# Performance work log

Hardware: AMD Instinct MI355X
Metric: run time of the kernel (lower is better)

Reference implementation:

```python
import jax, jax.numpy as jnp
from jax import lax
import numpy as np

K = 10            # size_feat
N_MU = 10         # number of mean-PSF components
NCH = K * K + N_MU  # 110 depthwise channels
KLEN = 65         # precomputed kernel length


def setup_inputs() -> dict:
    key = jax.random.key(0)
    ks = jax.random.split(key, 12)
    B, C, H, W = 1, 3, 256, 256
    img = jax.random.uniform(ks[0], (B, C, H, W), jnp.float32)
    zernike = jax.random.normal(ks[1], (B, H, W, 35), jnp.float32)
    # pos displacements (first 2 channels) scaled to a few pixels
    zernike = zernike.at[..., :2].multiply(2.0)
    fc1_w = jax.random.normal(ks[2], (200, 33), jnp.float32) / np.float32(np.sqrt(33))
    fc1_b = jax.random.normal(ks[3], (200,), jnp.float32) * 0.01
    fc2_w = jax.random.normal(ks[4], (200, 200), jnp.float32) / np.float32(np.sqrt(200))
    fc2_b = jax.random.normal(ks[5], (200,), jnp.float32) * 0.01
    fc3_w = jax.random.normal(ks[6], (100, 200), jnp.float32) * 0.01
    fc3_b = jnp.zeros((100,), jnp.float32)
    basis_left = jax.random.normal(ks[7], (KLEN, K), jnp.float32) * 0.05
    basis_right = jax.random.normal(ks[8], (KLEN, K), jnp.float32) * 0.05
    mu = jax.random.uniform(ks[9], (KLEN, N_MU), jnp.float32) / np.float32(KLEN)
    return dict(img=img, zernike=zernike, fc1_w=fc1_w, fc1_b=fc1_b,
                fc2_w=fc2_w, fc2_b=fc2_b, fc3_w=fc3_w, fc3_b=fc3_b,
                basis_left=basis_left, basis_right=basis_right, mu=mu, ksize=65)


def _grid_sample_border(img, pos):
    """Bilinear grid_sample, padding_mode='border', align_corners=False.
    img: (B,C,H,W), pos: (B,H,W,2) pixel displacements (x,y)."""
    B, C, H, W = img.shape
    yy, xx = jnp.meshgrid(jnp.arange(H, dtype=jnp.float32),
                          jnp.arange(W, dtype=jnp.float32), indexing='ij')
    grid = jnp.stack((xx, yy), -1)                       # (H,W,2)
    wh = jnp.array([W - 1, H - 1], jnp.float32)
    flow = 2.0 * (grid[None] + pos) / wh - 1.0           # (B,H,W,2) in [-1,1]
    ix = ((flow[..., 0] + 1.0) * W - 1.0) * 0.5
    iy = ((flow[..., 1] + 1.0) * H - 1.0) * 0.5
    ix = jnp.clip(ix, 0.0, W - 1)
    iy = jnp.clip(iy, 0.0, H - 1)
    x0 = jnp.floor(ix); y0 = jnp.floor(iy)
    wx = ix - x0;       wy = iy - y0
    x0i = jnp.clip(x0.astype(jnp.int32), 0, W - 1)
    y0i = jnp.clip(y0.astype(jnp.int32), 0, H - 1)
    x1i = jnp.clip(x0i + 1, 0, W - 1)
    y1i = jnp.clip(y0i + 1, 0, H - 1)

    def bilerp(im, x0i, x1i, y0i, y1i, wx, wy):
        g = lambda yi, xi: im[:, yi, xi]                 # (C,H,W)
        top = g(y0i, x0i) * (1 - wx) + g(y0i, x1i) * wx
        bot = g(y1i, x0i) * (1 - wx) + g(y1i, x1i) * wx
        return top * (1 - wy) + bot * wy

    return jax.vmap(bilerp)(img, x0i, x1i, y0i, y1i, wx, wy)


def _depthwise(x, w, pad_axis, pad):
    # x: (N, NCH, H, W); w: (NCH,1,kh,kw). Reflect 'same' padding on pad_axis.
    cfg = [(0, 0)] * 4
    cfg[pad_axis] = (pad, pad)
    xp = jnp.pad(x, cfg, mode='reflect')
    return lax.conv_general_dilated(
        xp, w, (1, 1), 'VALID',
        dimension_numbers=('NCHW', 'OIHW', 'NCHW'),
        feature_group_count=x.shape[1])


def _forward(img, zernike, fc1_w, fc1_b, fc2_w, fc2_b, fc3_w, fc3_b,
             basis_left, basis_right, mu, ksize):
    B, C, H, W = img.shape
    pad = ksize // 2
    # --- grid-sample warp ---
    tilt = _grid_sample_border(img, zernike[..., :2])    # (B,C,H,W)
    # --- per-pixel MLP -> PSF coefficients ---
    f = zernike[..., 2:]                                  # (B,H,W,33)
    h = jax.nn.leaky_relu(f @ fc1_w.T + fc1_b)
    h = jax.nn.leaky_relu(h @ fc2_w.T + fc2_b)
    coef = h @ fc3_w.T + fc3_b                            # (B,H,W,100)
    weight = jnp.concatenate(
        [coef, jnp.ones((B, H, W, N_MU), coef.dtype)], -1)  # (B,H,W,110)
    # --- elementwise weight multiply ---
    big = jnp.concatenate([tilt, jnp.ones_like(tilt)], 1)  # (B,2C,H,W)
    big = big[..., None] * weight[:, None]                 # (B,2C,H,W,110)
    x = big.reshape(B * 2 * C, H, W, NCH).transpose(0, 3, 1, 2)  # (B*2C,110,H,W)
    # --- separable depthwise blur kernels (outer products Z_i x X_j + mu) ---
    wl = jnp.concatenate([jnp.repeat(basis_left.T, K, axis=0), mu.T], 0)  # (110,klen)
    wr = jnp.concatenate([jnp.tile(basis_right.T, (K, 1)), mu.T], 0)      # (110,klen)
    wl = wl[:, None, :, None]                              # (110,1,klen,1)
    wr = wr[:, None, None, :]                              # (110,1,1,klen)
    y = _depthwise(x, wl, 2, pad)
    y = _depthwise(y, wr, 3, pad)
    d = y.reshape(B, 2 * C, NCH, H, W)
    out = jnp.sum(d[:, :3], axis=2) / jnp.sum(d[:, 3:], axis=2)  # (B,3,H,W)
    return out


def reference(img, zernike, fc1_w, fc1_b, fc2_w, fc2_b, fc3_w, fc3_b,
              basis_left, basis_right, mu, ksize):
    return _forward(img, zernike, fc1_w, fc1_b, fc2_w, fc2_b, fc3_w, fc3_b,
                    basis_left, basis_right, mu, ksize)
```

## Files before the change

### kernel.cpp

```cpp
#include <hip/hip_runtime.h>

#define HW 65536

typedef __attribute__((ext_vector_type(8))) short short8;
typedef __attribute__((ext_vector_type(4))) float float4v;

__device__ __forceinline__ int refl(int i){ if (i < 0) i = -i; if (i > 255) i = 510 - i; return i; }
__device__ __forceinline__ float lrelu(float x){ return x > 0.f ? x : 0.01f * x; }
__device__ __forceinline__ unsigned int f2bf(float x){
  union { float f; unsigned int u; } v; v.f = x;
  unsigned int r = v.u + 0x7fff + ((v.u >> 16) & 1);
  return r >> 16;
}

__global__ __launch_bounds__(256) void k_gridsample(const float* __restrict__ img,
                                                    const float* __restrict__ zern,
                                                    float* __restrict__ tilt){
  int x = threadIdx.x, y = blockIdx.x;
  int pix = y * 256 + x;
  float px = zern[pix * 35 + 0], py = zern[pix * 35 + 1];
  float ix = ((float)x + px) * (256.f / 255.f) - 0.5f;
  float iy = ((float)y + py) * (256.f / 255.f) - 0.5f;
  ix = fminf(fmaxf(ix, 0.f), 255.f);
  iy = fminf(fmaxf(iy, 0.f), 255.f);
  float x0f = floorf(ix), y0f = floorf(iy);
  float wx = ix - x0f, wy = iy - y0f;
  int x0 = (int)x0f, y0 = (int)y0f;
  int x1 = min(x0 + 1, 255), y1 = min(y0 + 1, 255);
  #pragma unroll
  for (int c = 0; c < 3; ++c){
    const float* im = img + c * HW;
    float g00 = im[y0 * 256 + x0], g01 = im[y0 * 256 + x1];
    float g10 = im[y1 * 256 + x0], g11 = im[y1 * 256 + x1];
    float top = g00 * (1.f - wx) + g01 * wx;
    float bot = g10 * (1.f - wx) + g11 * wx;
    tilt[c * HW + pix] = top * (1.f - wy) + bot * wy;
  }
}

#define W2OFF 13312
#define W3OFF 59904
__global__ __launch_bounds__(256) void k_wcvt(const float* __restrict__ w1,
    const float* __restrict__ w2, const float* __restrict__ w3,
    unsigned short* __restrict__ wbf){
  int i = blockIdx.x * 256 + threadIdx.x;
  if (i < 208 * 64){
    int n = i >> 6, k = i & 63;
    float v = (n < 200 && k < 33) ? w1[n * 33 + k] : 0.f;
    wbf[i] = (unsigned short)f2bf(v);
  } else if (i < W2OFF + 208 * 224){
    int j = i - W2OFF; int n = j / 224, k = j - n * 224;
    float v = (n < 200 && k < 200) ? w2[n * 200 + k] : 0.f;
    wbf[i] = (unsigned short)f2bf(v);
  } else if (i < 84992){
    int j = i - W3OFF; int n = j / 224, k = j - n * 224;
    float v = (n < 100 && k < 200) ? w3[n * 200 + k] : 0.f;
    wbf[i] = (unsigned short)f2bf(v);
  }
}

__global__ __launch_bounds__(256) void k_tz(const float* __restrict__ bl,
    const float* __restrict__ br, const float* __restrict__ mu,
    unsigned short* __restrict__ Tt){
  int e = blockIdx.x * 256 + threadIdx.x;
  if (e >= 46080) return;
  int t = e / 1536, rem = e - t * 1536;
  int m = rem / 96, k = rem - m * 96;
  int d = k - m;
  float v = 0.f;
  if (d >= 0 && d <= 64){
    if (t < 10)      v = bl[d * 10 + t];
    else if (t < 20) v = mu[d * 10 + (t - 10)];
    else             v = br[d * 10 + (t - 20)];
  }
  Tt[e] = (unsigned short)f2bf(v);
}

#define HSTR 232
__global__ __launch_bounds__(256) void k_mlp(const float* __restrict__ zern,
    const float* __restrict__ b1f, const float* __restrict__ b2f,
    const float* __restrict__ b3f, const unsigned short* __restrict__ wbf,
    float* __restrict__ coefp){
  __shared__ char smem[29696];
  unsigned short* H1 = (unsigned short*)smem;
  float*          H3 = (float*)smem;
  unsigned short* XB = (unsigned short*)(smem + 14848);
  unsigned short* H2 = XB;
  int tid = threadIdx.x;
  int pix0 = blockIdx.x * 32;
  int lane = tid & 63, wv = tid >> 6;
  int ln = lane & 15, qd = lane >> 4;

  for (int e = tid; e < 1152; e += 256) ((int*)XB)[e] = 0;
  for (int e = tid; e < 384; e += 256){
    int m = e / 12, j = e - m * 12;
    ((int*)H1)[m * 116 + 104 + j] = 0;
  }
  __syncthreads();
  for (int e = tid; e < 32 * 33; e += 256){
    int m = e / 33, k = e - m * 33;
    XB[m * 72 + k] = (unsigned short)f2bf(zern[(pix0 + m) * 35 + 2 + k]);
  }
  __syncthreads();

  for (int nt = wv; nt < 13; nt += 4){
    int n = nt * 16 + ln;
    short8 b0 = *(const short8*)(wbf + n * 64 + qd * 8);
    short8 b1 = *(const short8*)(wbf + n * 64 + 32 + qd * 8);
    float bv = (n < 200) ? b1f[n] : 0.f;
    #pragma unroll
    for (int mt = 0; mt < 2; ++mt){
      float4v acc = {bv, bv, bv, bv};
      short8 a0 = *(const short8*)(XB + (mt * 16 + ln) * 72 + qd * 8);
      short8 a1 = *(const short8*)(XB + (mt * 16 + ln) * 72 + 32 + qd * 8);
      acc = __builtin_amdgcn_mfma_f32_16x16x32_bf16(a0, b0, acc, 0, 0, 0);
      acc = __builtin_amdgcn_mfma_f32_16x16x32_bf16(a1, b1, acc, 0, 0, 0);
      #pragma unroll
      for (int r = 0; r < 4; ++r)
        H1[(mt * 16 + qd * 4 + r) * HSTR + n] = (unsigned short)f2bf(lrelu(acc[r]));
    }
  }
  __syncthreads();

  for (int e = tid; e < 384; e += 256){
    int m = e / 12, j = e - m * 12;
    ((int*)H2)[m * 116 + 104 + j] = 0;
  }
  {
    const unsigned short* w2p = wbf + W2OFF;
    for (int nt = wv; nt < 13; nt += 4){
      int n = nt * 16 + ln;
      short8 bf[7];
      #pragma unroll
      for (int kc = 0; kc < 7; ++kc)
        bf[kc] = *(const short8*)(w2p + n * 224 + kc * 32 + qd * 8);
      float bv = (n < 200) ? b2f[n] : 0.f;
      #pragma unroll
      for (int mt = 0; mt < 2; ++mt){
        float4v acc = {bv, bv, bv, bv};
        #pragma unroll
        for (int kc = 0; kc < 7; ++kc){
          short8 af = *(const short8*)(H1 + (mt * 16 + ln) * HSTR + kc * 32 + qd * 8);
          acc = __builtin_amdgcn_mfma_f32_16x16x32_bf16(af, bf[kc], acc, 0, 0, 0);
        }
        #pragma unroll
        for (int r = 0; r < 4; ++r)
          H2[(mt * 16 + qd * 4 + r) * HSTR + n] = (unsigned short)f2bf(lrelu(acc[r]));
      }
    }
  }
  __syncthreads();

  {
    const unsigned short* w3p = wbf + W3OFF;
    for (int nt = wv; nt < 7; nt += 4){
      int n = nt * 16 + ln;
      short8 bf[7];
      #pragma unroll
      for (int kc = 0; kc < 7; ++kc)
        bf[kc] = *(const short8*)(w3p + n * 224 + kc * 32 + qd * 8);
      float bv = (n < 100) ? b3f[n] : 0.f;
      #pragma unroll
      for (int mt = 0; mt < 2; ++mt){
        float4v acc = {bv, bv, bv, bv};
        #pragma unroll
        for (int kc = 0; kc < 7; ++kc){
          short8 af = *(const short8*)(H2 + (mt * 16 + ln) * HSTR + kc * 32 + qd * 8);
          acc = __builtin_amdgcn_mfma_f32_16x16x32_bf16(af, bf[kc], acc, 0, 0, 0);
        }
        #pragma unroll
        for (int r = 0; r < 4; ++r)
          H3[(mt * 16 + qd * 4 + r) * 113 + n] = acc[r];
      }
    }
  }
  __syncthreads();

  for (int e = tid; e < 3200; e += 256){
    int n = e >> 5, m = e & 31;
    coefp[n * HW + pix0 + m] = H3[m * 113 + n];
  }
}

#define VB 344
__global__ __launch_bounds__(256) void k_vconv10(const float* __restrict__ tilt,
    const float* __restrict__ coefp, const unsigned short* __restrict__ Tt,
    float* __restrict__ sbuf, float* __restrict__ smu){
  __shared__ __align__(16) unsigned short sxb[16 * VB];
  int tid = threadIdx.x;
  int bid = blockIdx.x;
  int lane = tid & 63, wv = tid >> 6;
  int ln = lane & 15, qd = lane >> 4;
  int col = tid & 15, seg = tid >> 4;
  int r0 = seg * 20;

  int goff[20];
  #pragma unroll
  for (int q = 0; q < 20; ++q) goff[q] = refl(r0 + q - 32) * 256 + col;

  for (int e = tid; e < 384; e += 256){
    int cc = e / 24, rp = e - cc * 24;
    sxb[cc * VB + 320 + rp] = 0;
  }

  if (bid < 640){
    int s = bid & 15;
    int cj = bid >> 4;
    int c = cj / 10, j = cj - c * 10;
    int x0 = s * 16;
    float treg[20];
    if (c < 3){
      const float* tc = tilt + c * HW + x0;
      #pragma unroll
      for (int q = 0; q < 20; ++q) treg[q] = tc[goff[q]];
    }
    float pf[20];
    {
      const float* cq = coefp + j * HW + x0;
      #pragma unroll
      for (int q = 0; q < 20; ++q) pf[q] = cq[goff[q]];
    }
    float4v acc[4];
    #pragma unroll
    for (int t = 0; t < 4; ++t) acc[t] = (float4v){0.f, 0.f, 0.f, 0.f};
    for (int i = 0; i < 10; ++i){
      __syncthreads();
      #pragma unroll
      for (int q = 0; q < 10; ++q){
        float v0 = pf[2 * q], v1 = pf[2 * q + 1];
        if (c < 3){ v0 *= treg[2 * q]; v1 *= treg[2 * q + 1]; }
        unsigned int pk = f2bf(v0) | (f2bf(v1) << 16);
        *(unsigned int*)&sxb[col * VB + r0 + 2 * q] = pk;
      }
      __syncthreads();
      if (i < 9){
        const float* cn = coefp + ((i + 1) * 10 + j) * HW + x0;
        #pragma unroll
        for (int q = 0; q < 20; ++q) pf[q] = cn[goff[q]];
      }
      const unsigned short* ta = Tt + i * 1536 + ln * 96 + qd * 8;
      short8 A0 = *(const short8*)(ta);
      short8 A1 = *(const short8*)(ta + 32);
      short8 A2 = *(const short8*)(ta + 64);
      #pragma unroll
      for (int t = 0; t < 4; ++t){
        int yt = wv * 4 + t;
        const unsigned short* bp = sxb + ln * VB + yt * 16 + qd * 8;
        short8 B0 = *(const short8*)(bp);
        short8 B1 = *(const short8*)(bp + 32);
        short8 B2 = *(const short8*)(bp + 64);
        acc[t] = __builtin_amdgcn_mfma_f32_16x16x32_bf16(A0, B0, acc[t], 0, 0, 0);
        acc[t] = __builtin_amdgcn_mfma_f32_16x16x32_bf16(A1, B1, acc[t], 0, 0, 0);
        acc[t] = __builtin_amdgcn_mfma_f32_16x16x32_bf16(A2, B2, acc[t], 0, 0, 0);
      }
    }
    float* S = sbuf + (c * 10 + j) * HW + x0 + ln;
    #pragma unroll
    for (int t = 0; t < 4; ++t){
      int yt = wv * 4 + t;
      #pragma unroll
      for (int r = 0; r < 4; ++r)
        S[(yt * 16 + qd * 4 + r) * 256] = acc[t][r];
    }
  } else {
    int b2 = bid - 640;
    int c = b2 >> 4, s = b2 & 15;
    int x0 = s * 16;
    const float* tc = tilt + c * HW + x0;
    float tv[20];
    #pragma unroll
    for (int q = 0; q < 20; ++q) tv[q] = tc[goff[q]];
    #pragma unroll
    for (int q = 0; q < 10; ++q){
      unsigned int pk = f2bf(tv[2 * q]) | (f2bf(tv[2 * q + 1]) << 16);
      *(unsigned int*)&sxb[col * VB + r0 + 2 * q] = pk;
    }
    __syncthreads();
    for (int m = 0; m < 10; ++m){
      const unsigned short* ta = Tt + (10 + m) * 1536 + ln * 96 + qd * 8;
      short8 A0 = *(const short8*)(ta);
      short8 A1 = *(const short8*)(ta + 32);
      short8 A2 = *(const short8*)(ta + 64);
      float4v acc[4];
      #pragma unroll
      for (int t = 0; t < 4; ++t) acc[t] = (float4v){0.f, 0.f, 0.f, 0.f};
      #pragma unroll
      for (int t = 0; t < 4; ++t){
        int yt = wv * 4 + t;
        const unsigned short* bp = sxb + ln * VB + yt * 16 + qd * 8;
        short8 B0 = *(const short8*)(bp);
        short8 B1 = *(const short8*)(bp + 32);
        short8 B2 = *(const short8*)(bp + 64);
        acc[t] = __builtin_amdgcn_mfma_f32_16x16x32_bf16(A0, B0, acc[t], 0, 0, 0);
        acc[t] = __builtin_amdgcn_mfma_f32_16x16x32_bf16(A1, B1, acc[t], 0, 0, 0);
        acc[t] = __builtin_amdgcn_mfma_f32_16x16x32_bf16(A2, B2, acc[t], 0, 0, 0);
      }
      float* S = smu + (c * 10 + m) * HW + x0 + ln;
      #pragma unroll
      for (int t = 0; t < 4; ++t){
        int yt = wv * 4 + t;
        #pragma unroll
        for (int r = 0; r < 4; ++r)
          S[(yt * 16 + qd * 4 + r) * 256] = acc[t][r];
      }
    }
  }
}

#define HS2 328
__global__ __launch_bounds__(256) void k_hconv8(const float* __restrict__ sbuf,
    const float* __restrict__ smu, const unsigned short* __restrict__ Tt,
    float* __restrict__ part){
  __shared__ __align__(16) unsigned short sxb[16 * HS2];
  int tid = threadIdx.x;
  int grp = blockIdx.x >> 4;
  int yt  = blockIdx.x & 15;
  int y0 = yt * 16;
  int lane = tid & 63, wv = tid >> 6;
  int ln = lane & 15, qd = lane >> 4;
  int srow = tid >> 4, scol = tid & 15;
  int isbr = (grp < 8);
  int tgt, h;
  if (isbr){ tgt = grp >> 1; h = grp & 1; }
  else     { int g2 = grp - 8; tgt = g2 >> 1; h = g2 & 1; }
  const float* base = isbr ? (sbuf + tgt * 10 * HW) : (smu + tgt * 10 * HW);
  int tbase = isbr ? 20 : 10;

  int gx[20];
  #pragma unroll
  for (int q = 0; q < 20; ++q) gx[q] = refl(scol * 20 - 32 + q);

  float4v acc[4];
  #pragma unroll
  for (int t = 0; t < 4; ++t) acc[t] = (float4v){0.f, 0.f, 0.f, 0.f};

  for (int p = 0; p < 5; ++p){
    int col = h * 5 + p;
    const float* plane = base + col * HW + (y0 + srow) * 256;
    __syncthreads();
    float v[20];
    #pragma unroll
    for (int q = 0; q < 20; ++q) v[q] = plane[gx[q]];
    #pragma unroll
    for (int q = 0; q < 10; ++q){
      unsigned int pk = f2bf(v[2 * q]) | (f2bf(v[2 * q + 1]) << 16);
      *(unsigned int*)&sxb[srow * HS2 + scol * 20 + 2 * q] = pk;
    }
    __syncthreads();
    const unsigned short* ta = Tt + (tbase + col) * 1536 + ln * 96 + qd * 8;
    short8 A0 = *(const short8*)(ta);
    short8 A1 = *(const short8*)(ta + 32);
    short8 A2 = *(const short8*)(ta + 64);
    #pragma unroll
    for (int t = 0; t < 4; ++t){
      int wt = wv * 4 + t;
      const unsigned short* bp = sxb + ln * HS2 + wt * 16 + qd * 8;
      short8 B0 = *(const short8*)(bp);
      short8 B1 = *(const short8*)(bp + 32);
      short8 B2 = *(const short8*)(bp + 64);
      acc[t] = __builtin_amdgcn_mfma_f32_16x16x32_bf16(A0, B0, acc[t], 0, 0, 0);
      acc[t] = __builtin_amdgcn_mfma_f32_16x16x32_bf16(A1, B1, acc[t], 0, 0, 0);
      acc[t] = __builtin_amdgcn_mfma_f32_16x16x32_bf16(A2, B2, acc[t], 0, 0, 0);
    }
  }
  #pragma unroll
  for (int t = 0; t < 4; ++t){
    int wt = wv * 4 + t;
    float4 res = {acc[t][0], acc[t][1], acc[t][2], acc[t][3]};
    *(float4*)(part + grp * HW + (y0 + ln) * 256 + wt * 16 + qd * 4) = res;
  }
}

__global__ __launch_bounds__(256) void k_final(const float* __restrict__ part,
                                               const float* __restrict__ mu,
                                               float* __restrict__ out){
  int pix = blockIdx.x * 256 + threadIdx.x;
  float muC = 0.f;
  #pragma unroll
  for (int m = 0; m < 10; ++m){
    float s = 0.f;
    for (int u = 0; u < 65; ++u) s += mu[u * 10 + m];
    muC += s * s;
  }
  float den = part[6 * HW + pix] + part[7 * HW + pix] + muC;
  float inv = 1.f / den;
  #pragma unroll
  for (int c = 0; c < 3; ++c){
    float num = part[(2 * c) * HW + pix] + part[(2 * c + 1) * HW + pix]
              + part[(8 + 2 * c) * HW + pix] + part[(9 + 2 * c) * HW + pix];
    out[c * HW + pix] = num * inv;
  }
}

extern "C" void kernel_launch(void* const* d_in, const int* in_sizes, int n_in,
                              void* d_out, int out_size, void* d_ws, size_t ws_size,
                              hipStream_t stream) {
  const float* img  = (const float*)d_in[0];
  const float* zern = (const float*)d_in[1];
  const float* w1   = (const float*)d_in[2];
  const float* b1   = (const float*)d_in[3];
  const float* w2   = (const float*)d_in[4];
  const float* b2   = (const float*)d_in[5];
  const float* w3   = (const float*)d_in[6];
  const float* b3   = (const float*)d_in[7];
  const float* bl   = (const float*)d_in[8];
  const float* br   = (const float*)d_in[9];
  const float* mu   = (const float*)d_in[10];
  float* out = (float*)d_out;

  float* w     = (float*)d_ws;
  float* tilt  = w;
  float* coefp = w + 3 * HW;
  float* part  = w + 3 * HW;
  float* sbuf  = w + 103 * HW;
  float* smu   = w + 143 * HW;
  unsigned short* wbf = (unsigned short*)sbuf;
  unsigned short* Tt  = (unsigned short*)(w + 173 * HW);

  k_gridsample<<<256, 256, 0, stream>>>(img, zern, tilt);
  k_wcvt<<<332, 256, 0, stream>>>(w1, w2, w3, wbf);
  k_tz<<<180, 256, 0, stream>>>(bl, br, mu, Tt);
  k_mlp<<<2048, 256, 0, stream>>>(zern, b1, b2, b3, wbf, coefp);
  k_vconv10<<<688, 256, 0, stream>>>(tilt, coefp, Tt, sbuf, smu);
  k_hconv8<<<224, 256, 0, stream>>>(sbuf, smu, Tt, part);
  k_final<<<256, 256, 0, stream>>>(part, mu, out);
}
```

Baseline: 170.9 us.

## Split vertical conv over i-halves and unroll horizontal conv per column plane

The vertical-conv kernel now splits the 10-term i reduction into two halves, each writing to a separate buffer, which doubles the block count from 640 to 1280. The horizontal-conv kernel sums the two half buffers on load and runs one plane per block instead of looping over five, raising the grid from 224 to 1120 blocks. The final kernel then reduces 10 partial planes per channel instead of 2. This raises parallelism and occupancy at the cost of extra intermediate buffers and more global traffic: an extra 40-plane buffer, double reads in hconv, and 70 plane reads in the final kernel.

```diff
diff --git a/kernel.cpp b/kernel.cpp
--- a/kernel.cpp
+++ b/kernel.cpp
@@ -183,9 +183,9 @@
 }
 
 #define VB 344
-__global__ __launch_bounds__(256) void k_vconv10(const float* __restrict__ tilt,
+__global__ __launch_bounds__(256) void k_vconv11(const float* __restrict__ tilt,
     const float* __restrict__ coefp, const unsigned short* __restrict__ Tt,
-    float* __restrict__ sbuf, float* __restrict__ smu){
+    float* __restrict__ sbufA, float* __restrict__ sbufB, float* __restrict__ smu){
   __shared__ __align__(16) unsigned short sxb[16 * VB];
   int tid = threadIdx.x;
   int bid = blockIdx.x;
@@ -203,10 +203,13 @@
     sxb[cc * VB + 320 + rp] = 0;
   }
 
-  if (bid < 640){
+  if (bid < 1280){
     int s = bid & 15;
-    int cj = bid >> 4;
-    int c = cj / 10, j = cj - c * 10;
+    int t = bid >> 4;
+    int c = t / 20;
+    int rem = t - c * 20;
+    int j = rem >> 1, ih = rem & 1;
+    int i0 = ih * 5;
     int x0 = s * 16;
     float treg[20];
     if (c < 3){
@@ -216,14 +219,15 @@
     }
     float pf[20];
     {
-      const float* cq = coefp + j * HW + x0;
+      const float* cq = coefp + (i0 * 10 + j) * HW + x0;
       #pragma unroll
       for (int q = 0; q < 20; ++q) pf[q] = cq[goff[q]];
     }
     float4v acc[4];
     #pragma unroll
-    for (int t = 0; t < 4; ++t) acc[t] = (float4v){0.f, 0.f, 0.f, 0.f};
-    for (int i = 0; i < 10; ++i){
+    for (int t2 = 0; t2 < 4; ++t2) acc[t2] = (float4v){0.f, 0.f, 0.f, 0.f};
+    for (int ii = 0; ii < 5; ++ii){
+      int i = i0 + ii;
       __syncthreads();
       #pragma unroll
       for (int q = 0; q < 10; ++q){
@@ -233,7 +237,7 @@
         *(unsigned int*)&sxb[col * VB + r0 + 2 * q] = pk;
       }
       __syncthreads();
-      if (i < 9){
+      if (ii < 4){
         const float* cn = coefp + ((i + 1) * 10 + j) * HW + x0;
         #pragma unroll
         for (int q = 0; q < 20; ++q) pf[q] = cn[goff[q]];
@@ -243,27 +247,27 @@
       short8 A1 = *(const short8*)(ta + 32);
       short8 A2 = *(const short8*)(ta + 64);
       #pragma unroll
-      for (int t = 0; t < 4; ++t){
-        int yt = wv * 4 + t;
+      for (int t2 = 0; t2 < 4; ++t2){
+        int yt = wv * 4 + t2;
         const unsigned short* bp = sxb + ln * VB + yt * 16 + qd * 8;
         short8 B0 = *(const short8*)(bp);
         short8 B1 = *(const short8*)(bp + 32);
         short8 B2 = *(const short8*)(bp + 64);
-        acc[t] = __builtin_amdgcn_mfma_f32_16x16x32_bf16(A0, B0, acc[t], 0, 0, 0);
-        acc[t] = __builtin_amdgcn_mfma_f32_16x16x32_bf16(A1, B1, acc[t], 0, 0, 0);
-        acc[t] = __builtin_amdgcn_mfma_f32_16x16x32_bf16(A2, B2, acc[t], 0, 0, 0);
-      }
-    }
-    float* S = sbuf + (c * 10 + j) * HW + x0 + ln;
-    #pragma unroll
-    for (int t = 0; t < 4; ++t){
-      int yt = wv * 4 + t;
+        acc[t2] = __builtin_amdgcn_mfma_f32_16x16x32_bf16(A0, B0, acc[t2], 0, 0, 0);
+        acc[t2] = __builtin_amdgcn_mfma_f32_16x16x32_bf16(A1, B1, acc[t2], 0, 0, 0);
+        acc[t2] = __builtin_amdgcn_mfma_f32_16x16x32_bf16(A2, B2, acc[t2], 0, 0, 0);
+      }
+    }
+    float* S = (ih ? sbufB : sbufA) + (c * 10 + j) * HW + x0 + ln;
+    #pragma unroll
+    for (int t2 = 0; t2 < 4; ++t2){
+      int yt = wv * 4 + t2;
       #pragma unroll
       for (int r = 0; r < 4; ++r)
-        S[(yt * 16 + qd * 4 + r) * 256] = acc[t][r];
+        S[(yt * 16 + qd * 4 + r) * 256] = acc[t2][r];
     }
   } else {
-    int b2 = bid - 640;
+    int b2 = bid - 1280;
     int c = b2 >> 4, s = b2 & 15;
     int x0 = s * 16;
     const float* tc = tilt + c * HW + x0;
@@ -283,34 +287,34 @@
       short8 A2 = *(const short8*)(ta + 64);
       float4v acc[4];
       #pragma unroll
-      for (int t = 0; t < 4; ++t) acc[t] = (float4v){0.f, 0.f, 0.f, 0.f};
-      #pragma unroll
-      for (int t = 0; t < 4; ++t){
-        int yt = wv * 4 + t;
+      for (int t2 = 0; t2 < 4; ++t2) acc[t2] = (float4v){0.f, 0.f, 0.f, 0.f};
+      #pragma unroll
+      for (int t2 = 0; t2 < 4; ++t2){
+        int yt = wv * 4 + t2;
         const unsigned short* bp = sxb + ln * VB + yt * 16 + qd * 8;
         short8 B0 = *(const short8*)(bp);
         short8 B1 = *(const short8*)(bp + 32);
         short8 B2 = *(const short8*)(bp + 64);
-        acc[t] = __builtin_amdgcn_mfma_f32_16x16x32_bf16(A0, B0, acc[t], 0, 0, 0);
-        acc[t] = __builtin_amdgcn_mfma_f32_16x16x32_bf16(A1, B1, acc[t], 0, 0, 0);
-        acc[t] = __builtin_amdgcn_mfma_f32_16x16x32_bf16(A2, B2, acc[t], 0, 0, 0);
+        acc[t2] = __builtin_amdgcn_mfma_f32_16x16x32_bf16(A0, B0, acc[t2], 0, 0, 0);
+        acc[t2] = __builtin_amdgcn_mfma_f32_16x16x32_bf16(A1, B1, acc[t2], 0, 0, 0);
+        acc[t2] = __builtin_amdgcn_mfma_f32_16x16x32_bf16(A2, B2, acc[t2], 0, 0, 0);
       }
       float* S = smu + (c * 10 + m) * HW + x0 + ln;
       #pragma unroll
-      for (int t = 0; t < 4; ++t){
-        int yt = wv * 4 + t;
+      for (int t2 = 0; t2 < 4; ++t2){
+        int yt = wv * 4 + t2;
         #pragma unroll
         for (int r = 0; r < 4; ++r)
-          S[(yt * 16 + qd * 4 + r) * 256] = acc[t][r];
-      }
-    }
-  }
-}
-
-#define HS2 328
-__global__ __launch_bounds__(256) void k_hconv8(const float* __restrict__ sbuf,
-    const float* __restrict__ smu, const unsigned short* __restrict__ Tt,
-    float* __restrict__ part){
+          S[(yt * 16 + qd * 4 + r) * 256] = acc[t2][r];
+      }
+    }
+  }
+}
+
+#define HS2 344
+__global__ __launch_bounds__(256) void k_hconv9(const float* __restrict__ sbufA,
+    const float* __restrict__ sbufB, const float* __restrict__ smu,
+    const unsigned short* __restrict__ Tt, float* __restrict__ part2){
   __shared__ __align__(16) unsigned short sxb[16 * HS2];
   int tid = threadIdx.x;
   int grp = blockIdx.x >> 4;
@@ -319,59 +323,57 @@
   int lane = tid & 63, wv = tid >> 6;
   int ln = lane & 15, qd = lane >> 4;
   int srow = tid >> 4, scol = tid & 15;
-  int isbr = (grp < 8);
-  int tgt, h;
-  if (isbr){ tgt = grp >> 1; h = grp & 1; }
-  else     { int g2 = grp - 8; tgt = g2 >> 1; h = g2 & 1; }
-  const float* base = isbr ? (sbuf + tgt * 10 * HW) : (smu + tgt * 10 * HW);
-  int tbase = isbr ? 20 : 10;
+
+  for (int e = tid; e < 384; e += 256){
+    int rr = e / 24, cp = e - rr * 24;
+    sxb[rr * HS2 + 320 + cp] = 0;
+  }
 
   int gx[20];
   #pragma unroll
   for (int q = 0; q < 20; ++q) gx[q] = refl(scol * 20 - 32 + q);
 
-  float4v acc[4];
-  #pragma unroll
-  for (int t = 0; t < 4; ++t) acc[t] = (float4v){0.f, 0.f, 0.f, 0.f};
-
-  for (int p = 0; p < 5; ++p){
-    int col = h * 5 + p;
-    const float* plane = base + col * HW + (y0 + srow) * 256;
-    __syncthreads();
-    float v[20];
-    #pragma unroll
-    for (int q = 0; q < 20; ++q) v[q] = plane[gx[q]];
+  if (grp < 40){
+    const float* pa = sbufA + grp * HW + (y0 + srow) * 256;
+    const float* pb = sbufB + grp * HW + (y0 + srow) * 256;
     #pragma unroll
     for (int q = 0; q < 10; ++q){
-      unsigned int pk = f2bf(v[2 * q]) | (f2bf(v[2 * q + 1]) << 16);
-      *(unsigned int*)&sxb[srow * HS2 + scol * 20 + 2 * q] = pk;
-    }
-    __syncthreads();
-    const unsigned short* ta = Tt + (tbase + col) * 1536 + ln * 96 + qd * 8;
-    short8 A0 = *(const short8*)(ta);
-    short8 A1 = *(const short8*)(ta + 32);
-    short8 A2 = *(const short8*)(ta + 64);
-    #pragma unroll
-    for (int t = 0; t < 4; ++t){
-      int wt = wv * 4 + t;
-      const unsigned short* bp = sxb + ln * HS2 + wt * 16 + qd * 8;
-      short8 B0 = *(const short8*)(bp);
-      short8 B1 = *(const short8*)(bp + 32);
-      short8 B2 = *(const short8*)(bp + 64);
-      acc[t] = __builtin_amdgcn_mfma_f32_16x16x32_bf16(A0, B0, acc[t], 0, 0, 0);
-      acc[t] = __builtin_amdgcn_mfma_f32_16x16x32_bf16(A1, B1, acc[t], 0, 0, 0);
-      acc[t] = __builtin_amdgcn_mfma_f32_16x16x32_bf16(A2, B2, acc[t], 0, 0, 0);
-    }
-  }
+      float v0 = pa[gx[2 * q]]     + pb[gx[2 * q]];
+      float v1 = pa[gx[2 * q + 1]] + pb[gx[2 * q + 1]];
+      *(unsigned int*)&sxb[srow * HS2 + scol * 20 + 2 * q] = f2bf(v0) | (f2bf(v1) << 16);
+    }
+  } else {
+    const float* pm = smu + (grp - 40) * HW + (y0 + srow) * 256;
+    #pragma unroll
+    for (int q = 0; q < 10; ++q){
+      float v0 = pm[gx[2 * q]], v1 = pm[gx[2 * q + 1]];
+      *(unsigned int*)&sxb[srow * HS2 + scol * 20 + 2 * q] = f2bf(v0) | (f2bf(v1) << 16);
+    }
+  }
+  __syncthreads();
+  int colk = (grp < 40) ? (grp % 10) : ((grp - 40) % 10);
+  int tbase = (grp < 40) ? 20 : 10;
+  const unsigned short* ta = Tt + (tbase + colk) * 1536 + ln * 96 + qd * 8;
+  short8 A0 = *(const short8*)(ta);
+  short8 A1 = *(const short8*)(ta + 32);
+  short8 A2 = *(const short8*)(ta + 64);
   #pragma unroll
   for (int t = 0; t < 4; ++t){
     int wt = wv * 4 + t;
-    float4 res = {acc[t][0], acc[t][1], acc[t][2], acc[t][3]};
-    *(float4*)(part + grp * HW + (y0 + ln) * 256 + wt * 16 + qd * 4) = res;
-  }
-}
-
-__global__ __launch_bounds__(256) void k_final(const float* __restrict__ part,
+    const unsigned short* bp = sxb + ln * HS2 + wt * 16 + qd * 8;
+    short8 B0 = *(const short8*)(bp);
+    short8 B1 = *(const short8*)(bp + 32);
+    short8 B2 = *(const short8*)(bp + 64);
+    float4v acc = {0.f, 0.f, 0.f, 0.f};
+    acc = __builtin_amdgcn_mfma_f32_16x16x32_bf16(A0, B0, acc, 0, 0, 0);
+    acc = __builtin_amdgcn_mfma_f32_16x16x32_bf16(A1, B1, acc, 0, 0, 0);
+    acc = __builtin_amdgcn_mfma_f32_16x16x32_bf16(A2, B2, acc, 0, 0, 0);
+    float4 res = {acc[0], acc[1], acc[2], acc[3]};
+    *(float4*)(part2 + grp * HW + (y0 + ln) * 256 + wt * 16 + qd * 4) = res;
+  }
+}
+
+__global__ __launch_bounds__(256) void k_final(const float* __restrict__ part2,
                                                const float* __restrict__ mu,
                                                float* __restrict__ out){
   int pix = blockIdx.x * 256 + threadIdx.x;
@@ -382,13 +384,17 @@
     for (int u = 0; u < 65; ++u) s += mu[u * 10 + m];
     muC += s * s;
   }
-  float den = part[6 * HW + pix] + part[7 * HW + pix] + muC;
+  float den = muC;
+  #pragma unroll
+  for (int q = 0; q < 10; ++q) den += part2[(30 + q) * HW + pix];
   float inv = 1.f / den;
   #pragma unroll
   for (int c = 0; c < 3; ++c){
-    float num = part[(2 * c) * HW + pix] + part[(2 * c + 1) * HW + pix]
-              + part[(8 + 2 * c) * HW + pix] + part[(9 + 2 * c) * HW + pix];
-    out[c * HW + pix] = num * inv;
+    float s = 0.f;
+    #pragma unroll
+    for (int q = 0; q < 10; ++q)
+      s += part2[(c * 10 + q) * HW + pix] + part2[(40 + c * 10 + q) * HW + pix];
+    out[c * HW + pix] = s * inv;
   }
 }
 
@@ -411,17 +417,18 @@
   float* w     = (float*)d_ws;
   float* tilt  = w;
   float* coefp = w + 3 * HW;
-  float* part  = w + 3 * HW;
-  float* sbuf  = w + 103 * HW;
-  float* smu   = w + 143 * HW;
-  unsigned short* wbf = (unsigned short*)sbuf;
-  unsigned short* Tt  = (unsigned short*)(w + 173 * HW);
+  float* part2 = w + 3 * HW;
+  float* sbufA = w + 103 * HW;
+  float* sbufB = w + 143 * HW;
+  float* smu   = w + 183 * HW;
+  unsigned short* wbf = (unsigned short*)sbufA;
+  unsigned short* Tt  = (unsigned short*)(w + 213 * HW);
 
   k_gridsample<<<256, 256, 0, stream>>>(img, zern, tilt);
   k_wcvt<<<332, 256, 0, stream>>>(w1, w2, w3, wbf);
   k_tz<<<180, 256, 0, stream>>>(bl, br, mu, Tt);
   k_mlp<<<2048, 256, 0, stream>>>(zern, b1, b2, b3, wbf, coefp);
-  k_vconv10<<<688, 256, 0, stream>>>(tilt, coefp, Tt, sbuf, smu);
-  k_hconv8<<<224, 256, 0, stream>>>(sbuf, smu, Tt, part);
-  k_final<<<256, 256, 0, stream>>>(part, mu, out);
-}
+  k_vconv11<<<1328, 256, 0, stream>>>(tilt, coefp, Tt, sbufA, sbufB, smu);
+  k_hconv9<<<1120, 256, 0, stream>>>(sbufA, sbufB, smu, Tt, part2);
+  k_final<<<256, 256, 0, stream>>>(part2, mu, out);
+}
```

Measured after the change: 184.4 us. +7.9%, slower.

## Merge prep kernels, double-buffer vconv LDS, and pad hconv LDS tail

Applied to the files above, without the earlier changes.

Merges the weight conversion and Toeplitz-matrix setup kernels into a single launch, which removes one kernel launch. In the vertical convolution, the LDS staging buffer is now double-buffered so one of the two __syncthreads per iteration can be dropped, at the cost of twice the shared memory per block. The horizontal conv LDS stride is widened and its tail columns zeroed, which appears to fix reads past the written region and changes the bank layout.

```diff
diff --git a/kernel.cpp b/kernel.cpp
--- a/kernel.cpp
+++ b/kernel.cpp
@@ -40,40 +40,39 @@
 
 #define W2OFF 13312
 #define W3OFF 59904
-__global__ __launch_bounds__(256) void k_wcvt(const float* __restrict__ w1,
+__global__ __launch_bounds__(256) void k_prep(const float* __restrict__ w1,
     const float* __restrict__ w2, const float* __restrict__ w3,
-    unsigned short* __restrict__ wbf){
+    const float* __restrict__ bl, const float* __restrict__ br,
+    const float* __restrict__ mu, unsigned short* __restrict__ wbf,
+    unsigned short* __restrict__ Tt){
   int i = blockIdx.x * 256 + threadIdx.x;
-  if (i < 208 * 64){
-    int n = i >> 6, k = i & 63;
-    float v = (n < 200 && k < 33) ? w1[n * 33 + k] : 0.f;
-    wbf[i] = (unsigned short)f2bf(v);
-  } else if (i < W2OFF + 208 * 224){
-    int j = i - W2OFF; int n = j / 224, k = j - n * 224;
-    float v = (n < 200 && k < 200) ? w2[n * 200 + k] : 0.f;
-    wbf[i] = (unsigned short)f2bf(v);
-  } else if (i < 84992){
-    int j = i - W3OFF; int n = j / 224, k = j - n * 224;
-    float v = (n < 100 && k < 200) ? w3[n * 200 + k] : 0.f;
-    wbf[i] = (unsigned short)f2bf(v);
-  }
-}
-
-__global__ __launch_bounds__(256) void k_tz(const float* __restrict__ bl,
-    const float* __restrict__ br, const float* __restrict__ mu,
-    unsigned short* __restrict__ Tt){
-  int e = blockIdx.x * 256 + threadIdx.x;
-  if (e >= 46080) return;
-  int t = e / 1536, rem = e - t * 1536;
-  int m = rem / 96, k = rem - m * 96;
-  int d = k - m;
-  float v = 0.f;
-  if (d >= 0 && d <= 64){
-    if (t < 10)      v = bl[d * 10 + t];
-    else if (t < 20) v = mu[d * 10 + (t - 10)];
-    else             v = br[d * 10 + (t - 20)];
-  }
-  Tt[e] = (unsigned short)f2bf(v);
+  if (i < 84992){
+    if (i < 208 * 64){
+      int n = i >> 6, k = i & 63;
+      float v = (n < 200 && k < 33) ? w1[n * 33 + k] : 0.f;
+      wbf[i] = (unsigned short)f2bf(v);
+    } else if (i < W2OFF + 208 * 224){
+      int j = i - W2OFF; int n = j / 224, k = j - n * 224;
+      float v = (n < 200 && k < 200) ? w2[n * 200 + k] : 0.f;
+      wbf[i] = (unsigned short)f2bf(v);
+    } else {
+      int j = i - W3OFF; int n = j / 224, k = j - n * 224;
+      float v = (n < 100 && k < 200) ? w3[n * 200 + k] : 0.f;
+      wbf[i] = (unsigned short)f2bf(v);
+    }
+  } else {
+    int e = i - 84992;
+    int t = e / 1536, rem = e - t * 1536;
+    int m = rem / 96, k = rem - m * 96;
+    int d = k - m;
+    float v = 0.f;
+    if (d >= 0 && d <= 64){
+      if (t < 10)      v = bl[d * 10 + t];
+      else if (t < 20) v = mu[d * 10 + (t - 10)];
+      else             v = br[d * 10 + (t - 20)];
+    }
+    Tt[e] = (unsigned short)f2bf(v);
+  }
 }
 
 #define HSTR 232
@@ -183,10 +182,10 @@
 }
 
 #define VB 344
-__global__ __launch_bounds__(256) void k_vconv10(const float* __restrict__ tilt,
+__global__ __launch_bounds__(256) void k_vconv13(const float* __restrict__ tilt,
     const float* __restrict__ coefp, const unsigned short* __restrict__ Tt,
     float* __restrict__ sbuf, float* __restrict__ smu){
-  __shared__ __align__(16) unsigned short sxb[16 * VB];
+  __shared__ __align__(16) unsigned short sxb[2][16 * VB];
   int tid = threadIdx.x;
   int bid = blockIdx.x;
   int lane = tid & 63, wv = tid >> 6;
@@ -198,9 +197,10 @@
   #pragma unroll
   for (int q = 0; q < 20; ++q) goff[q] = refl(r0 + q - 32) * 256 + col;
 
-  for (int e = tid; e < 384; e += 256){
-    int cc = e / 24, rp = e - cc * 24;
-    sxb[cc * VB + 320 + rp] = 0;
+  for (int e = tid; e < 768; e += 256){
+    int b = e / 384, r = e - b * 384;
+    int cc = r / 24, rp = r - cc * 24;
+    sxb[b][cc * VB + 320 + rp] = 0;
   }
 
   if (bid < 640){
@@ -224,13 +224,13 @@
     #pragma unroll
     for (int t = 0; t < 4; ++t) acc[t] = (float4v){0.f, 0.f, 0.f, 0.f};
     for (int i = 0; i < 10; ++i){
-      __syncthreads();
+      int us = i & 1;
+      unsigned short* sb = sxb[us];
       #pragma unroll
       for (int q = 0; q < 10; ++q){
         float v0 = pf[2 * q], v1 = pf[2 * q + 1];
         if (c < 3){ v0 *= treg[2 * q]; v1 *= treg[2 * q + 1]; }
-        unsigned int pk = f2bf(v0) | (f2bf(v1) << 16);
-        *(unsigned int*)&sxb[col * VB + r0 + 2 * q] = pk;
+        *(unsigned int*)&sb[col * VB + r0 + 2 * q] = f2bf(v0) | (f2bf(v1) << 16);
       }
       __syncthreads();
       if (i < 9){
@@ -245,7 +245,7 @@
       #pragma unroll
       for (int t = 0; t < 4; ++t){
         int yt = wv * 4 + t;
-        const unsigned short* bp = sxb + ln * VB + yt * 16 + qd * 8;
+        const unsigned short* bp = sb + ln * VB + yt * 16 + qd * 8;
         short8 B0 = *(const short8*)(bp);
         short8 B1 = *(const short8*)(bp + 32);
         short8 B2 = *(const short8*)(bp + 64);
@@ -272,8 +272,7 @@
     for (int q = 0; q < 20; ++q) tv[q] = tc[goff[q]];
     #pragma unroll
     for (int q = 0; q < 10; ++q){
-      unsigned int pk = f2bf(tv[2 * q]) | (f2bf(tv[2 * q + 1]) << 16);
-      *(unsigned int*)&sxb[col * VB + r0 + 2 * q] = pk;
+      *(unsigned int*)&sxb[0][col * VB + r0 + 2 * q] = f2bf(tv[2 * q]) | (f2bf(tv[2 * q + 1]) << 16);
     }
     __syncthreads();
     for (int m = 0; m < 10; ++m){
@@ -287,7 +286,7 @@
       #pragma unroll
       for (int t = 0; t < 4; ++t){
         int yt = wv * 4 + t;
-        const unsigned short* bp = sxb + ln * VB + yt * 16 + qd * 8;
+        const unsigned short* bp = sxb[0] + ln * VB + yt * 16 + qd * 8;
         short8 B0 = *(const short8*)(bp);
         short8 B1 = *(const short8*)(bp + 32);
         short8 B2 = *(const short8*)(bp + 64);
@@ -307,7 +306,7 @@
   }
 }
 
-#define HS2 328
+#define HS2 344
 __global__ __launch_bounds__(256) void k_hconv8(const float* __restrict__ sbuf,
     const float* __restrict__ smu, const unsigned short* __restrict__ Tt,
     float* __restrict__ part){
@@ -326,6 +325,11 @@
   const float* base = isbr ? (sbuf + tgt * 10 * HW) : (smu + tgt * 10 * HW);
   int tbase = isbr ? 20 : 10;
 
+  for (int e = tid; e < 384; e += 256){
+    int rr = e / 24, cp = e - rr * 24;
+    sxb[rr * HS2 + 320 + cp] = 0;
+  }
+
   int gx[20];
   #pragma unroll
   for (int q = 0; q < 20; ++q) gx[q] = refl(scol * 20 - 32 + q);
@@ -343,8 +347,8 @@
     for (int q = 0; q < 20; ++q) v[q] = plane[gx[q]];
     #pragma unroll
     for (int q = 0; q < 10; ++q){
-      unsigned int pk = f2bf(v[2 * q]) | (f2bf(v[2 * q + 1]) << 16);
-      *(unsigned int*)&sxb[srow * HS2 + scol * 20 + 2 * q] = pk;
+      *(unsigned int*)&sxb[srow * HS2 + scol * 20 + 2 * q] =
+          f2bf(v[2 * q]) | (f2bf(v[2 * q + 1]) << 16);
     }
     __syncthreads();
     const unsigned short* ta = Tt + (tbase + col) * 1536 + ln * 96 + qd * 8;
@@ -418,10 +422,9 @@
   unsigned short* Tt  = (unsigned short*)(w + 173 * HW);
 
   k_gridsample<<<256, 256, 0, stream>>>(img, zern, tilt);
-  k_wcvt<<<332, 256, 0, stream>>>(w1, w2, w3, wbf);
-  k_tz<<<180, 256, 0, stream>>>(bl, br, mu, Tt);
+  k_prep<<<512, 256, 0, stream>>>(w1, w2, w3, bl, br, mu, wbf, Tt);
   k_mlp<<<2048, 256, 0, stream>>>(zern, b1, b2, b3, wbf, coefp);
-  k_vconv10<<<688, 256, 0, stream>>>(tilt, coefp, Tt, sbuf, smu);
+  k_vconv13<<<688, 256, 0, stream>>>(tilt, coefp, Tt, sbuf, smu);
   k_hconv8<<<224, 256, 0, stream>>>(sbuf, smu, Tt, part);
   k_final<<<256, 256, 0, stream>>>(part, mu, out);
 }
```

New measurement: 169.8 us. No clear change (-0.7%).
